# Kernel optimization log

Hardware: AMD Instinct MI355X
Metric: run time of the kernel (lower is better)

The kernel has to match this reference:

```python
import jax, jax.numpy as jnp
import numpy as np

N_SRC, N_DST = 20000, 20000
N = N_SRC + N_DST            # homogeneous node count
E = 320000                   # bipartite edges
H, D, IN = 8, 16, 128        # heads, per-head dim, input dim
TEM = 0.7
NEG_SLOPE = 0.2              # DGL GATConv leaky_relu slope
E_NEG = E - int(round(E * 0.01))  # drop-edge keeps 316800 edges


def setup_inputs() -> dict:
    key = jax.random.key(0)
    ks = jax.random.split(key, 6)
    feat = jax.random.normal(ks[0], (N, IN), jnp.float32)
    edge_src = jax.random.randint(ks[1], (E,), 0, N_SRC, dtype=jnp.int32)
    edge_dst = jax.random.randint(ks[2], (E,), 0, N_DST, dtype=jnp.int32) + N_SRC
    rng = np.random.default_rng(0)
    neg_idx = jnp.asarray(np.sort(rng.permutation(E)[:E_NEG]).astype(np.int32))
    fc_w = jax.random.normal(ks[3], (IN, H * D), jnp.float32) / np.sqrt(IN).astype(np.float32)
    attn_l = jax.random.normal(ks[4], (H, D), jnp.float32) * 0.1
    attn_r = jax.random.normal(ks[5], (H, D), jnp.float32) * 0.1
    bias = jnp.zeros((H * D,), jnp.float32)
    prelu_a = jnp.full((1,), 0.25, jnp.float32)
    return dict(feat=feat, fc_w=fc_w, attn_l=attn_l, attn_r=attn_r, bias=bias,
                prelu_a=prelu_a, edge_src=edge_src, edge_dst=edge_dst, neg_idx=neg_idx)


def _gat(feat, fc_w, attn_l, attn_r, bias, prelu_a, src, dst):
    """DGL GATConv (attn_drop=0, bias=True, activation=PReLU) + self-loops, then head-mean."""
    loop = jnp.arange(N, dtype=src.dtype)
    src = jnp.concatenate([src, loop])
    dst = jnp.concatenate([dst, loop])
    z = (feat @ fc_w).reshape(N, H, D)                 # [N,H,D]
    el = jnp.sum(z * attn_l[None], axis=-1)            # [N,H]
    er = jnp.sum(z * attn_r[None], axis=-1)            # [N,H]
    e = el[src] + er[dst]                              # [E',H]
    e = jnp.where(e >= 0, e, NEG_SLOPE * e)            # leaky_relu
    # segment (edge) softmax over incoming edges of each dst node
    m = jax.ops.segment_max(e, dst, num_segments=N)
    w = jnp.exp(e - m[dst])
    denom = jax.ops.segment_sum(w, dst, num_segments=N)
    alpha = w / denom[dst]                             # [E',H]
    msg = alpha[:, :, None] * z[src]                   # [E',H,D]
    rst = jax.ops.segment_sum(msg, dst, num_segments=N)  # [N,H,D]
    rst = rst + bias.reshape(1, H, D)
    rst = jnp.where(rst >= 0, rst, prelu_a[0] * rst)   # PReLU (single param)
    return jnp.mean(rst, axis=1)                       # [N,D] head-mean


def reference(feat, fc_w, attn_l, attn_r, bias, prelu_a, edge_src, edge_dst, neg_idx):
    h = _gat(feat, fc_w, attn_l, attn_r, bias, prelu_a, edge_src, edge_dst)
    h_neg_full = _gat(feat, fc_w, attn_l, attn_r, bias, prelu_a,
                      edge_src[neg_idx], edge_dst[neg_idx])
    # predict-type (dst) nodes are ids [N_SRC, N)
    h_pos = h[N_SRC:]
    h_neg = h_neg_full[N_SRC:]
    eps = 1e-8
    num = jnp.sum(h_pos * h_neg, axis=-1)
    na = jnp.maximum(jnp.linalg.norm(h_pos, axis=-1), eps)
    nb = jnp.maximum(jnp.linalg.norm(h_neg, axis=-1), eps)
    cos = num / (na * nb)                              # F.cosine_similarity
    loss = jnp.log(jnp.sum(jnp.exp(cos / TEM)))
    return loss, h_pos
```

## Files before the change

kernel.cpp:

```cpp
#include <hip/hip_runtime.h>

#define NSRC 20000
#define NDST 20000
#define NTOT 40000
#define ETOT 320000
#define ENEG 316800
#define NH 8
#define ND 16
#define NHD 128
#define BCAP 64
#define BSTRIDE 136

typedef __bf16 v8bf __attribute__((ext_vector_type(8)));
typedef float v4f __attribute__((ext_vector_type(4)));


__global__ __launch_bounds__(256) void k_front(const float* __restrict__ A,
                                               const float* __restrict__ B,
                                               const float* __restrict__ attn_l,
                                               const float* __restrict__ attn_r,
                                               const int* __restrict__ neg_idx,
                                               unsigned short* __restrict__ z,
                                               float* __restrict__ el,
                                               float* __restrict__ er,
                                               unsigned char* __restrict__ flag) {
    const int tid = threadIdx.x;
    const int bid = blockIdx.x;
    if (bid >= 625) {
        int t0 = (bid - 625) * 256 + tid;
        for (int i = t0; i < ENEG; i += 32768) flag[neg_idx[i]] = 1;
        return;
    }
    __shared__ __bf16 Bs[128 * BSTRIDE];
    for (int i = tid; i < 4096; i += 256) {
        float4 v = ((const float4*)B)[i];
        int k = (i * 4) >> 7;
        int n = (i * 4) & 127;
        Bs[(n + 0) * BSTRIDE + k] = (__bf16)v.x;
        Bs[(n + 1) * BSTRIDE + k] = (__bf16)v.y;
        Bs[(n + 2) * BSTRIDE + k] = (__bf16)v.z;
        Bs[(n + 3) * BSTRIDE + k] = (__bf16)v.w;
    }
    __syncthreads();
    const int w = tid >> 6, lane = tid & 63;
    const int ml = lane & 15, q = lane >> 4;
    const int gm = bid * 64 + w * 16 + ml;
    v4f acc[8];
#pragma unroll
    for (int n = 0; n < 8; ++n) acc[n] = (v4f){0.f, 0.f, 0.f, 0.f};
#pragma unroll
    for (int ks = 0; ks < 4; ++ks) {
        const int k0 = ks * 32 + q * 8;
        float4 f0 = *(const float4*)(A + (size_t)gm * 128 + k0);
        float4 f1 = *(const float4*)(A + (size_t)gm * 128 + k0 + 4);
        v8bf av;
        av[0] = (__bf16)f0.x; av[1] = (__bf16)f0.y;
        av[2] = (__bf16)f0.z; av[3] = (__bf16)f0.w;
        av[4] = (__bf16)f1.x; av[5] = (__bf16)f1.y;
        av[6] = (__bf16)f1.z; av[7] = (__bf16)f1.w;
#pragma unroll
        for (int n = 0; n < 8; ++n) {
            v8bf bv = *(const v8bf*)(&Bs[(n * 16 + ml) * BSTRIDE + k0]);
            acc[n] = __builtin_amdgcn_mfma_f32_16x16x32_bf16(av, bv, acc[n], 0, 0, 0);
        }
    }
    const int rowbase = bid * 64 + w * 16 + q * 4;
#pragma unroll
    for (int n = 0; n < 8; ++n) {
        float alv = attn_l[n * 16 + ml];
        float arv = attn_r[n * 16 + ml];
#pragma unroll
        for (int r = 0; r < 4; ++r) {
            float v = acc[n][r];
            unsigned int u = __float_as_uint(v);
            unsigned int b = (u + 0x7fffu + ((u >> 16) & 1u)) >> 16;
            z[(size_t)(rowbase + r) * NHD + n * 16 + ml] = (unsigned short)b;
            float pl = v * alv, pr = v * arv;
#pragma unroll
            for (int s = 1; s <= 8; s <<= 1) {
                pl += __shfl_xor(pl, s, 64);
                pr += __shfl_xor(pr, s, 64);
            }
            if (ml == 0) {
                el[(rowbase + r) * NH + n] = pl;
                er[(rowbase + r) * NH + n] = pr;
            }
        }
    }
}

__global__ __launch_bounds__(256) void k_scatter(const int* __restrict__ edge_src,
                                                 const int* __restrict__ edge_dst,
                                                 const unsigned char* __restrict__ flag,
                                                 int* __restrict__ cursor,
                                                 int* __restrict__ csr) {
    int i = blockIdx.x * 256 + threadIdx.x;
    if (i >= ETOT) return;
    int d = edge_dst[i] - NSRC;
    int slot = atomicAdd(&cursor[d], 1);
    int v = edge_src[i];
    if (flag[i]) v |= (int)0x80000000u;
    if (slot < BCAP) csr[d * BCAP + slot] = v;
}

__global__ __launch_bounds__(256) void k_agg(const int* __restrict__ degarr,
                                             const int* __restrict__ csr,
                                             const unsigned short* __restrict__ z,
                                             const float* __restrict__ el,
                                             const float* __restrict__ er,
                                             const float* __restrict__ bias,
                                             const float* __restrict__ prelu_a,
                                             float* __restrict__ out,
                                             float* __restrict__ expcos) {
    const int lane = threadIdx.x & 63;
    const int wid = threadIdx.x >> 6;
    const int d = (blockIdx.x << 2) + wid;

    const int g = NSRC + d;
    const int hl = lane >> 3;
    const int j8 = lane & 7;
    const int rs = d * BCAP;
    const int deg = degarr[d];
    const float erd = er[g * NH + hl];
    const float aslope = prelu_a[0];
    const float NEGINF = -__builtin_inff();

    float mF = NEGINF, lF = 0.f, lN = 0.f;
    float aF0 = 0.f, aF1 = 0.f, aN0 = 0.f, aN1 = 0.f;

    for (int base = 0; base < deg; base += 16) {
        const int j0 = base + j8, j1 = base + 8 + j8;
        int ent0 = (j0 < deg) ? csr[rs + j0] : g;
        int ent1 = (j1 < deg) ? csr[rs + j1] : g;
        unsigned int zr[16];
#pragma unroll
        for (int jj = 0; jj < 16; ++jj) {
            int entry = __shfl((jj < 8) ? ent0 : ent1, jj & 7, 64);
            zr[jj] = *(const unsigned int*)(z + ((size_t)(entry & 0x7FFFFFFF) << 7) + 2 * lane);
        }
        float e0 = el[(size_t)(ent0 & 0x7FFFFFFF) * NH + hl] + erd;
        float e1 = el[(size_t)(ent1 & 0x7FFFFFFF) * NH + hl] + erd;
        e0 = (e0 >= 0.f) ? e0 : 0.2f * e0;
        e1 = (e1 >= 0.f) ? e1 : 0.2f * e1;
        float ev0 = (j0 < deg) ? e0 : NEGINF;
        float ev1 = (j1 < deg) ? e1 : NEGINF;
        const int fl0 = (j0 < deg) && (ent0 < 0);
        const int fl1 = (j1 < deg) && (ent1 < 0);
        float cm = fmaxf(ev0, ev1);
#pragma unroll
        for (int s = 1; s <= 4; s <<= 1) cm = fmaxf(cm, __shfl_xor(cm, s, 64));
        float nm = fmaxf(mF, cm);
        float sc = (nm == mF) ? 1.f : __expf(mF - nm);
        mF = nm;
        float wf0 = __expf(ev0 - mF);
        float wf1 = __expf(ev1 - mF);
        lF = lF * sc + wf0 + wf1;
        lN = lN * sc + (fl0 ? wf0 : 0.f) + (fl1 ? wf1 : 0.f);
        float w0 = fl0 ? -wf0 : wf0;
        float w1 = fl1 ? -wf1 : wf1;
        aF0 *= sc; aF1 *= sc; aN0 *= sc; aN1 *= sc;
#pragma unroll
        for (int jj = 0; jj < 16; ++jj) {
            float v = __shfl((jj < 8) ? w0 : w1, (lane & 56) | (jj & 7), 64);
            float wf = fabsf(v);
            float wn = (v < 0.f) ? wf : 0.f;
            float zx = __uint_as_float(zr[jj] << 16);
            float zy = __uint_as_float(zr[jj] & 0xffff0000u);
            aF0 = fmaf(wf, zx, aF0);
            aF1 = fmaf(wf, zy, aF1);
            aN0 = fmaf(wn, zx, aN0);
            aN1 = fmaf(wn, zy, aN1);
        }
    }

    {
        float e = el[g * NH + hl] + erd;
        e = (e >= 0.f) ? e : 0.2f * e;
        float nm = fmaxf(mF, e);
        float sc = (nm == mF) ? 1.f : __expf(mF - nm);
        lF *= sc; lN *= sc;
        aF0 *= sc; aF1 *= sc; aN0 *= sc; aN1 *= sc;
        mF = nm;
        float wf = __expf(e - mF);
        if (j8 == 0) { lF += wf; lN += wf; }
        unsigned int zv = *(const unsigned int*)(z + ((size_t)g << 7) + 2 * lane);
        float zx = __uint_as_float(zv << 16);
        float zy = __uint_as_float(zv & 0xffff0000u);
        aF0 = fmaf(wf, zx, aF0);
        aF1 = fmaf(wf, zy, aF1);
        aN0 = fmaf(wf, zx, aN0);
        aN1 = fmaf(wf, zy, aN1);
    }

#pragma unroll
    for (int s = 1; s <= 4; s <<= 1) {
        lF += __shfl_xor(lF, s, 64);
        lN += __shfl_xor(lN, s, 64);
    }
    const int c0 = 2 * lane;
    float b0 = bias[c0], b1 = bias[c0 + 1];
    float rF0 = aF0 / lF + b0, rF1 = aF1 / lF + b1;
    float rN0 = aN0 / lN + b0, rN1 = aN1 / lN + b1;
    rF0 = (rF0 >= 0.f) ? rF0 : aslope * rF0;
    rF1 = (rF1 >= 0.f) ? rF1 : aslope * rF1;
    rN0 = (rN0 >= 0.f) ? rN0 : aslope * rN0;
    rN1 = (rN1 >= 0.f) ? rN1 : aslope * rN1;
#pragma unroll
    for (int s = 8; s <= 32; s <<= 1) {
        rF0 += __shfl_xor(rF0, s, 64);
        rF1 += __shfl_xor(rF1, s, 64);
        rN0 += __shfl_xor(rN0, s, 64);
        rN1 += __shfl_xor(rN1, s, 64);
    }
    float hF0 = rF0 * 0.125f, hF1 = rF1 * 0.125f;
    float hN0 = rN0 * 0.125f, hN1 = rN1 * 0.125f;
    if (lane < 8) {
        out[1 + d * ND + 2 * lane] = hF0;
        out[1 + d * ND + 2 * lane + 1] = hF1;
    }
    float num = hF0 * hN0 + hF1 * hN1;
    float na = hF0 * hF0 + hF1 * hF1;
    float nb = hN0 * hN0 + hN1 * hN1;
#pragma unroll
    for (int s = 1; s <= 4; s <<= 1) {
        num += __shfl_xor(num, s, 64);
        na += __shfl_xor(na, s, 64);
        nb += __shfl_xor(nb, s, 64);
    }
    if (lane == 0) {
        float cosv = num / (fmaxf(sqrtf(na), 1e-8f) * fmaxf(sqrtf(nb), 1e-8f));
        expcos[d] = __expf(cosv / 0.7f);
    }
}

__global__ __launch_bounds__(1024) void k_loss(const float* __restrict__ expcos,
                                               float* __restrict__ out) {
    __shared__ float sbuf[16];
    float s = 0.f;
    for (int i = threadIdx.x; i < NDST; i += 1024) s += expcos[i];
    for (int sh = 1; sh < 64; sh <<= 1) s += __shfl_xor(s, sh, 64);
    if ((threadIdx.x & 63) == 0) sbuf[threadIdx.x >> 6] = s;
    __syncthreads();
    if (threadIdx.x < 16) {
        float t = sbuf[threadIdx.x];
        for (int sh = 1; sh < 16; sh <<= 1) t += __shfl_xor(t, sh, 16);
        if (threadIdx.x == 0) out[0] = logf(t);
    }
}

extern "C" void kernel_launch(void* const* d_in, const int* in_sizes, int n_in,
                              void* d_out, int out_size, void* d_ws, size_t ws_size,
                              hipStream_t stream) {
    const float* feat = (const float*)d_in[0];
    const float* fc_w = (const float*)d_in[1];
    const float* attn_l = (const float*)d_in[2];
    const float* attn_r = (const float*)d_in[3];
    const float* bias = (const float*)d_in[4];
    const float* prelu_a = (const float*)d_in[5];
    const int* edge_src = (const int*)d_in[6];
    const int* edge_dst = (const int*)d_in[7];
    const int* neg_idx = (const int*)d_in[8];
    float* out = (float*)d_out;

    char* ws = (char*)d_ws;
    int* cursor = (int*)(ws + 0);
    unsigned char* flag = (unsigned char*)(ws + 80000);
    int* csr = (int*)(ws + 400000);
    float* expcos = (float*)(ws + 5520000);
    unsigned short* z = (unsigned short*)(ws + 5600000);
    float* el = (float*)(ws + 15840000);
    float* er = (float*)(ws + 17120000);

    hipMemsetAsync(d_ws, 0, 400000, stream);
    k_front<<<753, 256, 0, stream>>>(feat, fc_w, attn_l, attn_r, neg_idx,
                                     z, el, er, flag);
    k_scatter<<<(ETOT + 255) / 256, 256, 0, stream>>>(edge_src, edge_dst, flag,
                                                      cursor, csr);
    k_agg<<<NDST / 4, 256, 0, stream>>>(cursor, csr, z, el, er, bias, prelu_a,
                                        out, expcos);
    k_loss<<<1, 1024, 0, stream>>>(expcos, out);
}
```

Measured before the change: 157.5 us.

## Fuse loss reduction into aggregation, use bitset neg flags, widen edge batch

```diff
diff --git a/kernel.cpp b/kernel.cpp
--- a/kernel.cpp
+++ b/kernel.cpp
@@ -10,6 +10,7 @@
 #define NHD 128
 #define BCAP 64
 #define BSTRIDE 136
+#define NBLK_AGG (NDST / 4)
 
 typedef __bf16 v8bf __attribute__((ext_vector_type(8)));
 typedef float v4f __attribute__((ext_vector_type(4)));
@@ -23,12 +24,15 @@
                                                unsigned short* __restrict__ z,
                                                float* __restrict__ el,
                                                float* __restrict__ er,
-                                               unsigned char* __restrict__ flag) {
+                                               unsigned int* __restrict__ negbits) {
     const int tid = threadIdx.x;
     const int bid = blockIdx.x;
     if (bid >= 625) {
         int t0 = (bid - 625) * 256 + tid;
-        for (int i = t0; i < ENEG; i += 32768) flag[neg_idx[i]] = 1;
+        for (int i = t0; i < ENEG; i += 32768) {
+            int e = neg_idx[i];
+            atomicOr(&negbits[e >> 5], 1u << (e & 31));
+        }
         return;
     }
     __shared__ __bf16 Bs[128 * BSTRIDE];
@@ -91,7 +95,7 @@
 
 __global__ __launch_bounds__(256) void k_scatter(const int* __restrict__ edge_src,
                                                  const int* __restrict__ edge_dst,
-                                                 const unsigned char* __restrict__ flag,
+                                                 const unsigned int* __restrict__ negbits,
                                                  int* __restrict__ cursor,
                                                  int* __restrict__ csr) {
     int i = blockIdx.x * 256 + threadIdx.x;
@@ -99,7 +103,7 @@
     int d = edge_dst[i] - NSRC;
     int slot = atomicAdd(&cursor[d], 1);
     int v = edge_src[i];
-    if (flag[i]) v |= (int)0x80000000u;
+    if ((negbits[i >> 5] >> (i & 31)) & 1u) v |= (int)0x80000000u;
     if (slot < BCAP) csr[d * BCAP + slot] = v;
 }
 
@@ -111,8 +115,23 @@
                                              const float* __restrict__ bias,
                                              const float* __restrict__ prelu_a,
                                              float* __restrict__ out,
-                                             float* __restrict__ expcos) {
+                                             float* __restrict__ expcos,
+                                             unsigned int* __restrict__ donecnt) {
     const int lane = threadIdx.x & 63;
+    if (blockIdx.x == NBLK_AGG) {
+        if (threadIdx.x >= 64) return;
+        while (__hip_atomic_load(donecnt, __ATOMIC_ACQUIRE,
+                                 __HIP_MEMORY_SCOPE_AGENT) < NBLK_AGG)
+            __builtin_amdgcn_s_sleep(8);
+        float s = 0.f;
+        for (int i = lane; i < NDST; i += 64)
+            s += __hip_atomic_load(&expcos[i], __ATOMIC_RELAXED,
+                                   __HIP_MEMORY_SCOPE_AGENT);
+#pragma unroll
+        for (int sh = 1; sh < 64; sh <<= 1) s += __shfl_xor(s, sh, 64);
+        if (lane == 0) out[0] = logf(s);
+        return;
+    }
     const int wid = threadIdx.x >> 6;
     const int d = (blockIdx.x << 2) + wid;
 
@@ -128,11 +147,13 @@
     float mF = NEGINF, lF = 0.f, lN = 0.f;
     float aF0 = 0.f, aF1 = 0.f, aN0 = 0.f, aN1 = 0.f;
 
-    for (int base = 0; base < deg; base += 16) {
-        const int j0 = base + j8, j1 = base + 8 + j8;
+    for (int base = 0; base < deg; base += 32) {
+        const int j0 = base + j8, j1 = j0 + 8, j2 = j0 + 16, j3 = j0 + 24;
+        const bool half2 = (base + 16) < deg;
         int ent0 = (j0 < deg) ? csr[rs + j0] : g;
         int ent1 = (j1 < deg) ? csr[rs + j1] : g;
-        unsigned int zr[16];
+        int ent2 = g, ent3 = g;
+        unsigned int zr[32];
 #pragma unroll
         for (int jj = 0; jj < 16; ++jj) {
             int entry = __shfl((jj < 8) ? ent0 : ent1, jj & 7, 64);
@@ -140,13 +161,31 @@
         }
         float e0 = el[(size_t)(ent0 & 0x7FFFFFFF) * NH + hl] + erd;
         float e1 = el[(size_t)(ent1 & 0x7FFFFFFF) * NH + hl] + erd;
+        float e2 = NEGINF, e3 = NEGINF;
+        if (half2) {
+            ent2 = (j2 < deg) ? csr[rs + j2] : g;
+            ent3 = (j3 < deg) ? csr[rs + j3] : g;
+#pragma unroll
+            for (int jj = 16; jj < 32; ++jj) {
+                int entry = __shfl((jj < 24) ? ent2 : ent3, jj & 7, 64);
+                zr[jj] = *(const unsigned int*)(z + ((size_t)(entry & 0x7FFFFFFF) << 7) + 2 * lane);
+            }
+            e2 = el[(size_t)(ent2 & 0x7FFFFFFF) * NH + hl] + erd;
+            e3 = el[(size_t)(ent3 & 0x7FFFFFFF) * NH + hl] + erd;
+            e2 = (e2 >= 0.f) ? e2 : 0.2f * e2;
+            e3 = (e3 >= 0.f) ? e3 : 0.2f * e3;
+        }
         e0 = (e0 >= 0.f) ? e0 : 0.2f * e0;
         e1 = (e1 >= 0.f) ? e1 : 0.2f * e1;
         float ev0 = (j0 < deg) ? e0 : NEGINF;
         float ev1 = (j1 < deg) ? e1 : NEGINF;
+        float ev2 = (j2 < deg) ? e2 : NEGINF;
+        float ev3 = (j3 < deg) ? e3 : NEGINF;
         const int fl0 = (j0 < deg) && (ent0 < 0);
         const int fl1 = (j1 < deg) && (ent1 < 0);
-        float cm = fmaxf(ev0, ev1);
+        const int fl2 = (j2 < deg) && (ent2 < 0);
+        const int fl3 = (j3 < deg) && (ent3 < 0);
+        float cm = fmaxf(fmaxf(ev0, ev1), fmaxf(ev2, ev3));
 #pragma unroll
         for (int s = 1; s <= 4; s <<= 1) cm = fmaxf(cm, __shfl_xor(cm, s, 64));
         float nm = fmaxf(mF, cm);
@@ -154,10 +193,15 @@
         mF = nm;
         float wf0 = __expf(ev0 - mF);
         float wf1 = __expf(ev1 - mF);
-        lF = lF * sc + wf0 + wf1;
-        lN = lN * sc + (fl0 ? wf0 : 0.f) + (fl1 ? wf1 : 0.f);
+        float wf2 = __expf(ev2 - mF);
+        float wf3 = __expf(ev3 - mF);
+        lF = lF * sc + wf0 + wf1 + wf2 + wf3;
+        lN = lN * sc + (fl0 ? wf0 : 0.f) + (fl1 ? wf1 : 0.f) +
+             (fl2 ? wf2 : 0.f) + (fl3 ? wf3 : 0.f);
         float w0 = fl0 ? -wf0 : wf0;
         float w1 = fl1 ? -wf1 : wf1;
+        float w2 = fl2 ? -wf2 : wf2;
+        float w3 = fl3 ? -wf3 : wf3;
         aF0 *= sc; aF1 *= sc; aN0 *= sc; aN1 *= sc;
 #pragma unroll
         for (int jj = 0; jj < 16; ++jj) {
@@ -170,6 +214,20 @@
             aF1 = fmaf(wf, zy, aF1);
             aN0 = fmaf(wn, zx, aN0);
             aN1 = fmaf(wn, zy, aN1);
+        }
+        if (half2) {
+#pragma unroll
+            for (int jj = 16; jj < 32; ++jj) {
+                float v = __shfl((jj < 24) ? w2 : w3, (lane & 56) | (jj & 7), 64);
+                float wf = fabsf(v);
+                float wn = (v < 0.f) ? wf : 0.f;
+                float zx = __uint_as_float(zr[jj] << 16);
+                float zy = __uint_as_float(zr[jj] & 0xffff0000u);
+                aF0 = fmaf(wf, zx, aF0);
+                aF1 = fmaf(wf, zy, aF1);
+                aN0 = fmaf(wn, zx, aN0);
+                aN1 = fmaf(wn, zy, aN1);
+            }
         }
     }
 
@@ -231,20 +289,10 @@
         float cosv = num / (fmaxf(sqrtf(na), 1e-8f) * fmaxf(sqrtf(nb), 1e-8f));
         expcos[d] = __expf(cosv / 0.7f);
     }
-}
-
-__global__ __launch_bounds__(1024) void k_loss(const float* __restrict__ expcos,
-                                               float* __restrict__ out) {
-    __shared__ float sbuf[16];
-    float s = 0.f;
-    for (int i = threadIdx.x; i < NDST; i += 1024) s += expcos[i];
-    for (int sh = 1; sh < 64; sh <<= 1) s += __shfl_xor(s, sh, 64);
-    if ((threadIdx.x & 63) == 0) sbuf[threadIdx.x >> 6] = s;
     __syncthreads();
-    if (threadIdx.x < 16) {
-        float t = sbuf[threadIdx.x];
-        for (int sh = 1; sh < 16; sh <<= 1) t += __shfl_xor(t, sh, 16);
-        if (threadIdx.x == 0) out[0] = logf(t);
+    if (threadIdx.x == 0) {
+        __threadfence();
+        atomicAdd(donecnt, 1u);
     }
 }
 
@@ -263,20 +311,20 @@
     float* out = (float*)d_out;
 
     char* ws = (char*)d_ws;
-    int* cursor = (int*)(ws + 0);
-    unsigned char* flag = (unsigned char*)(ws + 80000);
-    int* csr = (int*)(ws + 400000);
-    float* expcos = (float*)(ws + 5520000);
-    unsigned short* z = (unsigned short*)(ws + 5600000);
-    float* el = (float*)(ws + 15840000);
-    float* er = (float*)(ws + 17120000);
-
-    hipMemsetAsync(d_ws, 0, 400000, stream);
+    unsigned int* donecnt = (unsigned int*)(ws + 0);
+    unsigned int* negbits = (unsigned int*)(ws + 64);
+    int* cursor = (int*)(ws + 40064);
+    int* csr = (int*)(ws + 120064);
+    float* expcos = (float*)(ws + 5240064);
+    unsigned short* z = (unsigned short*)(ws + 5320064);
+    float* el = (float*)(ws + 15560064);
+    float* er = (float*)(ws + 16840064);
+
+    hipMemsetAsync(d_ws, 0, 120064, stream);
     k_front<<<753, 256, 0, stream>>>(feat, fc_w, attn_l, attn_r, neg_idx,
-                                     z, el, er, flag);
-    k_scatter<<<(ETOT + 255) / 256, 256, 0, stream>>>(edge_src, edge_dst, flag,
-                                                      cursor, csr);
-    k_agg<<<NDST / 4, 256, 0, stream>>>(cursor, csr, z, el, er, bias, prelu_a,
-                                        out, expcos);
-    k_loss<<<1, 1024, 0, stream>>>(expcos, out);
+                                     z, el, er, negbits);
+    k_scatter<<<(ETOT + 255) / 256, 256, 0, stream>>>(edge_src, edge_dst,
+                                                      negbits, cursor, csr);
+    k_agg<<<NBLK_AGG + 1, 256, 0, stream>>>(cursor, csr, z, el, er, bias,
+                                            prelu_a, out, expcos, donecnt);
 }
```

Result: slower. 389.8 us (+147.5%).
